# Performance work log

Hardware: AMD Instinct MI355X
Metric: run time of the kernel (lower is better)

The kernel has to match this reference:

```python
import jax, jax.numpy as jnp
import numpy as np

B, S, DIN, DOUT, A, T, H = 8, 1024, 1024, 1024, 4, 4, 8  # arity A, T cell types, hidden H


def setup_inputs() -> dict:
    key = jax.random.key(0)
    ks = jax.random.split(key, 6)
    x = jax.random.normal(ks[0], (B, S, DIN), jnp.float32)
    sc = 1.0 / np.sqrt(DIN).astype(np.float32)
    weight = jax.random.uniform(ks[1], (A * DOUT, DIN), jnp.float32, -sc, sc)
    bias = jax.random.uniform(ks[2], (A * DOUT,), jnp.float32, -sc, sc)
    # stacked per-cell-type MLP params: arity -> H -> 1 (tanh)
    cw1 = jax.random.normal(ks[3], (T, A, H), jnp.float32) / np.sqrt(A).astype(np.float32)
    cb1 = jnp.zeros((T, H), jnp.float32)
    cw2 = jax.random.normal(ks[4], (T, H), jnp.float32) / np.sqrt(H).astype(np.float32)
    cb2 = jnp.zeros((T,), jnp.float32)
    return {"x": x, "weight": weight, "bias": bias,
            "cw1": cw1, "cb1": cb1, "cw2": cw2, "cb2": cb2}


def reference(x, weight, bias, cw1, cb1, cw2, cb2):
    T_, A_, H_ = cw1.shape
    Dout = weight.shape[0] // A_
    G = Dout // T_  # neurons per cell type (cell_indices = contiguous blocks via np.repeat)
    # all_inputs = F.linear(input, weight, bias): (B, S, A*Dout)
    z = jnp.einsum('bsd,od->bso', x, weight) + bias
    # slice per-neuron arity chunks -> (B, S, T, G, A)
    z = z.reshape(z.shape[0], z.shape[1], T_, G, A_)
    # per-cell-type MLP applied to every neuron of that type (replaces Python loop)
    h = jnp.tanh(jnp.einsum('bstga,tah->bstgh', z, cw1) + cb1[:, None, :])
    o = jnp.einsum('bstgh,th->bstg', h, cw2) + cb2[:, None]
    # concat over neurons -> (B, S, Dout)
    return o.reshape(o.shape[0], o.shape[1], Dout)
```

## Files before the change

kernel.cpp:

```cpp
#include <hip/hip_runtime.h>


typedef __bf16 bf16x8 __attribute__((ext_vector_type(8)));
typedef float f32x4 __attribute__((ext_vector_type(4)));
typedef float f32x16 __attribute__((ext_vector_type(16)));

#define BM 256
#define BN 256
#define BK 64
#define KDIM 1024
#define NT 16
#define BUFB 65536
#define BBASE 32768
#define ZS 260
#define XN8 (8192 * 1024 / 8)
#define WN8 (4096 * 1024 / 8)

__global__ __launch_bounds__(256) void cvt_bf16_kernel(
    const float* __restrict__ x, const float* __restrict__ w,
    __bf16* __restrict__ xb, __bf16* __restrict__ wb) {
    int i = blockIdx.x * 256 + threadIdx.x;
    const float* src;
    __bf16* dst;
    int j;
    if (i < XN8) { src = x; dst = xb; j = i; }
    else         { src = w; dst = wb; j = i - XN8; }
    const f32x4* p = (const f32x4*)src + 2 * (size_t)j;
    f32x4 a = p[0], b = p[1];
    bf16x8 o;
    o[0] = (__bf16)a[0]; o[1] = (__bf16)a[1]; o[2] = (__bf16)a[2]; o[3] = (__bf16)a[3];
    o[4] = (__bf16)b[0]; o[5] = (__bf16)b[1]; o[6] = (__bf16)b[2]; o[7] = (__bf16)b[3];
    ((bf16x8*)dst)[j] = o;
}

union __align__(16) SmemU {
    unsigned char raw[2 * BUFB];
    float z[64 * ZS];
};

#define FENCE() asm volatile("" ::: "memory")
#define BARRIER() do { FENCE(); __builtin_amdgcn_s_barrier(); FENCE(); } while (0)

__global__ __launch_bounds__(512, 2) void fused_gemm_mlp_kernel(
    const __bf16* __restrict__ Ag,
    const __bf16* __restrict__ Bg,
    const float* __restrict__ bias,
    const float* __restrict__ cw1,
    const float* __restrict__ cb1,
    const float* __restrict__ cw2,
    const float* __restrict__ cb2,
    float* __restrict__ out)
{
    __shared__ SmemU u;

    const int tid  = threadIdx.x;
    const int wave = tid >> 6;
    const int lane = tid & 63;
    const int wm = wave >> 2;
    const int wn = wave & 3;
    const int bn0 = blockIdx.x * BN;
    const int bm0 = blockIdx.y * BM;

    const int srow  = lane >> 3;
    const int scol8 = (((lane & 7) ^ srow) * 8);

    const int lr5 = lane & 31;
    const int lk2 = lane >> 5;
    const int lx  = lane & 7;
    const int lg  = lr5 >> 3;
    int aoff[4], boff[2], slot[4];
#pragma unroll
    for (int mi = 0; mi < 4; ++mi) aoff[mi] = (wm * 16 + mi * 4 + lg) * 1024 + lx * 128;
#pragma unroll
    for (int ni = 0; ni < 2; ++ni) boff[ni] = BBASE + (wn * 8 + ni * 4 + lg) * 1024 + lx * 128;
#pragma unroll
    for (int ks = 0; ks < 4; ++ks) slot[ks] = ((ks * 2 + lk2) ^ lx) * 16;

    const char* sb = (const char*)u.raw;

    auto stageA = [&](int t, int half) {
        if (t >= NT) return;
        const int dst = (t & 1) * BUFB + (half * 16 + wave * 2) * 1024;
        const __bf16* g = Ag + (size_t)(bm0 + half * 128 + wave * 16 + srow) * KDIM
                        + t * BK + scol8;
        __builtin_amdgcn_global_load_lds(
            (__attribute__((address_space(1))) void*)g,
            (__attribute__((address_space(3))) void*)&u.raw[dst], 16, 0, 0);
        __builtin_amdgcn_global_load_lds(
            (__attribute__((address_space(1))) void*)(g + 8 * KDIM),
            (__attribute__((address_space(3))) void*)&u.raw[dst + 1024], 16, 0, 0);
    };
    auto stageB = [&](int t, int half) {
        if (t >= NT) return;
        const int dst = (t & 1) * BUFB + BBASE + (half * 16 + wave * 2) * 1024;
        const __bf16* g = Bg + (size_t)(bn0 + half * 128 + wave * 16 + srow) * KDIM
                        + t * BK + scol8;
        __builtin_amdgcn_global_load_lds(
            (__attribute__((address_space(1))) void*)g,
            (__attribute__((address_space(3))) void*)&u.raw[dst], 16, 0, 0);
        __builtin_amdgcn_global_load_lds(
            (__attribute__((address_space(1))) void*)(g + 8 * KDIM),
            (__attribute__((address_space(3))) void*)&u.raw[dst + 1024], 16, 0, 0);
    };

    f32x16 acc[4][2] = {};
    bf16x8 aA[8];
    bf16x8 a1f[8];
    bf16x8 bf0[4], bf1[4];

    stageB(0, 0); stageB(0, 1); stageA(0, 0); stageA(0, 1); stageB(1, 0);
    asm volatile("s_waitcnt vmcnt(2)" ::: "memory");
    BARRIER();
#pragma unroll
    for (int mi = 0; mi < 2; ++mi)
#pragma unroll
        for (int ks = 0; ks < 4; ++ks)
            aA[mi * 4 + ks] = *(const bf16x8*)(sb + aoff[mi] + slot[ks]);
    stageB(1, 1);

#pragma unroll 2
    for (int T = 0; T < NT; ++T) {
        const int buf  = (T & 1) * BUFB;
        const int nbuf = buf ^ BUFB;

        BARRIER();
#pragma unroll
        for (int ks = 0; ks < 4; ++ks)
            bf0[ks] = *(const bf16x8*)(sb + buf + boff[0] + slot[ks]);
        stageA(T + 1, 0);
        __builtin_amdgcn_s_setprio(1);
#pragma unroll
        for (int mi = 0; mi < 2; ++mi)
#pragma unroll
            for (int ks = 0; ks < 4; ++ks)
                acc[mi][0] = __builtin_amdgcn_mfma_f32_32x32x16_bf16(
                    aA[mi * 4 + ks], bf0[ks], acc[mi][0], 0, 0, 0);
        __builtin_amdgcn_s_setprio(0);

        BARRIER();
#pragma unroll
        for (int ks = 0; ks < 4; ++ks)
            bf1[ks] = *(const bf16x8*)(sb + buf + boff[1] + slot[ks]);
        stageA(T + 1, 1);
        __builtin_amdgcn_s_setprio(1);
#pragma unroll
        for (int mi = 0; mi < 2; ++mi)
#pragma unroll
            for (int ks = 0; ks < 4; ++ks)
                acc[mi][1] = __builtin_amdgcn_mfma_f32_32x32x16_bf16(
                    aA[mi * 4 + ks], bf1[ks], acc[mi][1], 0, 0, 0);
        __builtin_amdgcn_s_setprio(0);

        BARRIER();
#pragma unroll
        for (int mi = 0; mi < 2; ++mi)
#pragma unroll
            for (int ks = 0; ks < 4; ++ks)
                a1f[mi * 4 + ks] = *(const bf16x8*)(sb + buf + aoff[2 + mi] + slot[ks]);
        stageB(T + 2, 0);
        __builtin_amdgcn_s_setprio(1);
#pragma unroll
        for (int mi = 0; mi < 2; ++mi)
#pragma unroll
            for (int ks = 0; ks < 4; ++ks)
                acc[2 + mi][0] = __builtin_amdgcn_mfma_f32_32x32x16_bf16(
                    a1f[mi * 4 + ks], bf0[ks], acc[2 + mi][0], 0, 0, 0);
        __builtin_amdgcn_s_setprio(0);
        asm volatile("s_waitcnt vmcnt(2)" ::: "memory");

        BARRIER();
        if (T + 1 < NT) {
#pragma unroll
            for (int mi = 0; mi < 2; ++mi)
#pragma unroll
                for (int ks = 0; ks < 4; ++ks)
                    aA[mi * 4 + ks] = *(const bf16x8*)(sb + nbuf + aoff[mi] + slot[ks]);
        }
        stageB(T + 2, 1);
        __builtin_amdgcn_s_setprio(1);
#pragma unroll
        for (int mi = 0; mi < 2; ++mi)
#pragma unroll
            for (int ks = 0; ks < 4; ++ks)
                acc[2 + mi][1] = __builtin_amdgcn_mfma_f32_32x32x16_bf16(
                    a1f[mi * 4 + ks], bf1[ks], acc[2 + mi][1], 0, 0, 0);
        __builtin_amdgcn_s_setprio(0);
    }

    const int tct = bn0 >> 10;
    float w1[32], b1[8], w2[8];
#pragma unroll
    for (int i = 0; i < 32; ++i) w1[i] = cw1[tct * 32 + i];
#pragma unroll
    for (int i = 0; i < 8; ++i) { b1[i] = cb1[tct * 8 + i]; w2[i] = cw2[tct * 8 + i]; }
    const float b2 = cb2[tct];

    float bcol[2];
#pragma unroll
    for (int ni = 0; ni < 2; ++ni)
        bcol[ni] = bias[bn0 + wn * 64 + ni * 32 + lr5];

    const float L2E2 = 2.885390081777927f;

    asm volatile("s_waitcnt vmcnt(0)" ::: "memory");
    __syncthreads();

#pragma unroll
    for (int h = 0; h < 4; ++h) {
        if (wm == (h >> 1)) {
            const int mi0 = (h & 1) * 2;
#pragma unroll
            for (int dmi = 0; dmi < 2; ++dmi) {
#pragma unroll
                for (int ni = 0; ni < 2; ++ni) {
                    const int n = wn * 64 + ni * 32 + lr5;
#pragma unroll
                    for (int g = 0; g < 4; ++g) {
                        const int rb = dmi * 32 + g * 8 + lk2 * 4;
                        u.z[(rb + 0) * ZS + n] = acc[mi0 + dmi][ni][g * 4 + 0] + bcol[ni];
                        u.z[(rb + 1) * ZS + n] = acc[mi0 + dmi][ni][g * 4 + 1] + bcol[ni];
                        u.z[(rb + 2) * ZS + n] = acc[mi0 + dmi][ni][g * 4 + 2] + bcol[ni];
                        u.z[(rb + 3) * ZS + n] = acc[mi0 + dmi][ni][g * 4 + 3] + bcol[ni];
                    }
                }
            }
        }
        __syncthreads();

#pragma unroll
        for (int it = 0; it < 8; ++it) {
            const int i = tid + it * 512;
            const int q = i & 63;
            const int r = i >> 6;
            f32x4 z4 = *(const f32x4*)&u.z[r * ZS + 4 * q];
            float o = 0.f;
#pragma unroll
            for (int hh = 0; hh < 8; ++hh) {
                float pre = z4[0] * w1[0 * 8 + hh] + z4[1] * w1[1 * 8 + hh]
                          + z4[2] * w1[2 * 8 + hh] + z4[3] * w1[3 * 8 + hh] + b1[hh];
                float e = __builtin_amdgcn_exp2f(pre * L2E2);
                float th = 1.0f - 2.0f * __builtin_amdgcn_rcpf(e + 1.0f);
                o += th * w2[hh];
            }
            o += b2;
            out[(size_t)(bm0 + h * 64 + r) * 1024 + (bn0 >> 2) + q] = o;
        }
        __syncthreads();
    }
}

extern "C" void kernel_launch(void* const* d_in, const int* in_sizes, int n_in,
                              void* d_out, int out_size, void* d_ws, size_t ws_size,
                              hipStream_t stream) {
    const float* x    = (const float*)d_in[0];
    const float* w    = (const float*)d_in[1];
    const float* bias = (const float*)d_in[2];
    const float* cw1  = (const float*)d_in[3];
    const float* cb1  = (const float*)d_in[4];
    const float* cw2  = (const float*)d_in[5];
    const float* cb2  = (const float*)d_in[6];
    float* out = (float*)d_out;

    __bf16* xb = (__bf16*)d_ws;
    __bf16* wb = xb + (size_t)8192 * 1024;

    cvt_bf16_kernel<<<(XN8 + WN8) / 256, 256, 0, stream>>>(x, w, xb, wb);

    dim3 grid(4096 / BN, 8192 / BM);
    fused_gemm_mlp_kernel<<<grid, 512, 0, stream>>>(xb, wb, bias, cw1, cb1, cw2, cb2, out);
}
```

Baseline: 195.8 us.

## Re-pipeline LDS fragment loads and pad epilogue z-tile to avoid bank conflicts

Reorders the main loop's LDS fragment loads so bf0 for the next tile is prefetched together with aA after the last barrier. The a1f load moves earlier into the second phase and bf1 into the first. A/B staging order in the prologue is swapped, and the final vmcnt wait is tightened on the last iterations. The epilogue z tile switches to a padded 5-wide-per-group layout (row stride 321) so the scattered stores and per-thread reads avoid LDS bank conflicts, at the cost of scalar instead of vector LDS reads.

```diff
diff --git a/kernel.cpp b/kernel.cpp
--- a/kernel.cpp
+++ b/kernel.cpp
@@ -12,7 +12,7 @@
 #define NT 16
 #define BUFB 65536
 #define BBASE 32768
-#define ZS 260
+#define RS 321
 #define XN8 (8192 * 1024 / 8)
 #define WN8 (4096 * 1024 / 8)
 
@@ -35,7 +35,7 @@
 
 union __align__(16) SmemU {
     unsigned char raw[2 * BUFB];
-    float z[64 * ZS];
+    float z[64 * RS];
 };
 
 #define FENCE() asm volatile("" ::: "memory")
@@ -108,7 +108,7 @@
     bf16x8 a1f[8];
     bf16x8 bf0[4], bf1[4];
 
-    stageB(0, 0); stageB(0, 1); stageA(0, 0); stageA(0, 1); stageB(1, 0);
+    stageA(0, 0); stageA(0, 1); stageB(0, 0); stageB(0, 1); stageB(1, 0);
     asm volatile("s_waitcnt vmcnt(2)" ::: "memory");
     BARRIER();
 #pragma unroll
@@ -116,6 +116,9 @@
 #pragma unroll
         for (int ks = 0; ks < 4; ++ks)
             aA[mi * 4 + ks] = *(const bf16x8*)(sb + aoff[mi] + slot[ks]);
+#pragma unroll
+    for (int ks = 0; ks < 4; ++ks)
+        bf0[ks] = *(const bf16x8*)(sb + boff[0] + slot[ks]);
     stageB(1, 1);
 
 #pragma unroll 2
@@ -126,7 +129,7 @@
         BARRIER();
 #pragma unroll
         for (int ks = 0; ks < 4; ++ks)
-            bf0[ks] = *(const bf16x8*)(sb + buf + boff[0] + slot[ks]);
+            bf1[ks] = *(const bf16x8*)(sb + buf + boff[1] + slot[ks]);
         stageA(T + 1, 0);
         __builtin_amdgcn_s_setprio(1);
 #pragma unroll
@@ -139,8 +142,10 @@
 
         BARRIER();
 #pragma unroll
-        for (int ks = 0; ks < 4; ++ks)
-            bf1[ks] = *(const bf16x8*)(sb + buf + boff[1] + slot[ks]);
+        for (int mi = 0; mi < 2; ++mi)
+#pragma unroll
+            for (int ks = 0; ks < 4; ++ks)
+                a1f[mi * 4 + ks] = *(const bf16x8*)(sb + buf + aoff[2 + mi] + slot[ks]);
         stageA(T + 1, 1);
         __builtin_amdgcn_s_setprio(1);
 #pragma unroll
@@ -152,11 +157,6 @@
         __builtin_amdgcn_s_setprio(0);
 
         BARRIER();
-#pragma unroll
-        for (int mi = 0; mi < 2; ++mi)
-#pragma unroll
-            for (int ks = 0; ks < 4; ++ks)
-                a1f[mi * 4 + ks] = *(const bf16x8*)(sb + buf + aoff[2 + mi] + slot[ks]);
         stageB(T + 2, 0);
         __builtin_amdgcn_s_setprio(1);
 #pragma unroll
@@ -166,7 +166,8 @@
                 acc[2 + mi][0] = __builtin_amdgcn_mfma_f32_32x32x16_bf16(
                     a1f[mi * 4 + ks], bf0[ks], acc[2 + mi][0], 0, 0, 0);
         __builtin_amdgcn_s_setprio(0);
-        asm volatile("s_waitcnt vmcnt(2)" ::: "memory");
+        if (T + 2 < NT) asm volatile("s_waitcnt vmcnt(2)" ::: "memory");
+        else            asm volatile("s_waitcnt vmcnt(0)" ::: "memory");
 
         BARRIER();
         if (T + 1 < NT) {
@@ -175,6 +176,9 @@
 #pragma unroll
                 for (int ks = 0; ks < 4; ++ks)
                     aA[mi * 4 + ks] = *(const bf16x8*)(sb + nbuf + aoff[mi] + slot[ks]);
+#pragma unroll
+            for (int ks = 0; ks < 4; ++ks)
+                bf0[ks] = *(const bf16x8*)(sb + nbuf + boff[0] + slot[ks]);
         }
         stageB(T + 2, 1);
         __builtin_amdgcn_s_setprio(1);
@@ -196,9 +200,13 @@
     const float b2 = cb2[tct];
 
     float bcol[2];
-#pragma unroll
-    for (int ni = 0; ni < 2; ++ni)
-        bcol[ni] = bias[bn0 + wn * 64 + ni * 32 + lr5];
+    int zc[2];
+#pragma unroll
+    for (int ni = 0; ni < 2; ++ni) {
+        const int n = wn * 64 + ni * 32 + lr5;
+        bcol[ni] = bias[bn0 + n];
+        zc[ni] = 5 * (n >> 2) + (n & 3);
+    }
 
     const float L2E2 = 2.885390081777927f;
 
@@ -213,14 +221,13 @@
             for (int dmi = 0; dmi < 2; ++dmi) {
 #pragma unroll
                 for (int ni = 0; ni < 2; ++ni) {
-                    const int n = wn * 64 + ni * 32 + lr5;
 #pragma unroll
                     for (int g = 0; g < 4; ++g) {
                         const int rb = dmi * 32 + g * 8 + lk2 * 4;
-                        u.z[(rb + 0) * ZS + n] = acc[mi0 + dmi][ni][g * 4 + 0] + bcol[ni];
-                        u.z[(rb + 1) * ZS + n] = acc[mi0 + dmi][ni][g * 4 + 1] + bcol[ni];
-                        u.z[(rb + 2) * ZS + n] = acc[mi0 + dmi][ni][g * 4 + 2] + bcol[ni];
-                        u.z[(rb + 3) * ZS + n] = acc[mi0 + dmi][ni][g * 4 + 3] + bcol[ni];
+                        u.z[(rb + 0) * RS + zc[ni]] = acc[mi0 + dmi][ni][g * 4 + 0] + bcol[ni];
+                        u.z[(rb + 1) * RS + zc[ni]] = acc[mi0 + dmi][ni][g * 4 + 1] + bcol[ni];
+                        u.z[(rb + 2) * RS + zc[ni]] = acc[mi0 + dmi][ni][g * 4 + 2] + bcol[ni];
+                        u.z[(rb + 3) * RS + zc[ni]] = acc[mi0 + dmi][ni][g * 4 + 3] + bcol[ni];
                     }
                 }
             }
@@ -232,12 +239,13 @@
             const int i = tid + it * 512;
             const int q = i & 63;
             const int r = i >> 6;
-            f32x4 z4 = *(const f32x4*)&u.z[r * ZS + 4 * q];
+            const float* zp = &u.z[r * RS + 5 * q];
+            const float z0 = zp[0], z1 = zp[1], z2 = zp[2], z3 = zp[3];
             float o = 0.f;
 #pragma unroll
             for (int hh = 0; hh < 8; ++hh) {
-                float pre = z4[0] * w1[0 * 8 + hh] + z4[1] * w1[1 * 8 + hh]
-                          + z4[2] * w1[2 * 8 + hh] + z4[3] * w1[3 * 8 + hh] + b1[hh];
+                float pre = z0 * w1[0 * 8 + hh] + z1 * w1[1 * 8 + hh]
+                          + z2 * w1[2 * 8 + hh] + z3 * w1[3 * 8 + hh] + b1[hh];
                 float e = __builtin_amdgcn_exp2f(pre * L2E2);
                 float th = 1.0f - 2.0f * __builtin_amdgcn_rcpf(e + 1.0f);
                 o += th * w2[hh];
```

After: 202.4 us. 3.4% more time.
